# Kernel optimization log

Measured on AMD Instinct MI355X. Metric: run time of the kernel, lower is better.

## Reference

```python
import jax, jax.numpy as jnp
import numpy as np

C_M, C_Z, C_H = 256, 128, 32
EPS = 1e-3      # outer-product-mean normalization eps
LN_EPS = 1e-5   # LayerNorm eps (torch default)


def setup_inputs() -> dict:
    key = jax.random.key(0)
    ks = jax.random.split(key, 8)
    B, S, R = 1, 128, 256
    m = jax.random.normal(ks[0], (B, S, R, C_M), dtype=jnp.float32)
    mask = jnp.ones((B, S, R), dtype=jnp.float32)
    ln_g = jnp.ones((C_M,), dtype=jnp.float32)
    ln_b = jnp.zeros((C_M,), dtype=jnp.float32)
    w1 = jax.random.normal(ks[1], (C_M, C_H), dtype=jnp.float32) * (1.0 / np.sqrt(C_M))
    b1 = jnp.zeros((C_H,), dtype=jnp.float32)
    w2 = jax.random.normal(ks[2], (C_M, C_H), dtype=jnp.float32) * (1.0 / np.sqrt(C_M))
    b2 = jnp.zeros((C_H,), dtype=jnp.float32)
    # linear_out uses init='final' (zeros) in training; use small random for a nontrivial baseline
    w_out = jax.random.normal(ks[3], (C_H * C_H, C_Z), dtype=jnp.float32) * 0.02
    b_out = jnp.zeros((C_Z,), dtype=jnp.float32)
    return {"m": m, "mask": mask, "ln_g": ln_g, "ln_b": ln_b,
            "w1": w1, "b1": b1, "w2": w2, "b2": b2,
            "w_out": w_out, "b_out": b_out}


def reference(m, mask, ln_g, ln_b, w1, b1, w2, b2, w_out, b_out):
    # LayerNorm over c_m
    mu = jnp.mean(m, axis=-1, keepdims=True)
    var = jnp.mean(jnp.square(m - mu), axis=-1, keepdims=True)
    mn = (m - mu) * jax.lax.rsqrt(var + LN_EPS) * ln_g + ln_b

    msk = mask[..., None]                       # [B,S,R,1]
    a = (mn @ w1 + b1) * msk                    # [B,S,R,h]
    b = (mn @ w2 + b2) * msk                    # [B,S,R,h]
    a = jnp.swapaxes(a, -2, -3)                 # [B,R,S,h]
    b = jnp.swapaxes(b, -2, -3)                 # [B,R,S,h]

    # outer product mean over the MSA (seq) dim: [B,R,R,h,h]
    outer = jnp.einsum('...isc,...jse->...ijce', a, b)
    outer = outer.reshape(*outer.shape[:-2], C_H * C_H)  # [B,R,R,h*h]
    outer = outer @ w_out + b_out               # [B,R,R,c_z]

    # normalization: pairwise count of valid MSA rows
    norm = jnp.einsum('...sia,...sja->...ija', msk, msk)  # [B,R,R,1]
    return outer / (EPS + norm)
```

## Files before the change

### kernel.cpp

```cpp
#include <hip/hip_runtime.h>

#define R   256
#define S   128
#define CM  256
#define CH  32
#define CZ  128

typedef __attribute__((ext_vector_type(8))) short short8;
typedef __attribute__((ext_vector_type(4))) float f32x4;
typedef unsigned short ushort_t;

__device__ inline ushort_t f2bf(float f) {
    union { float f; unsigned u; } v; v.f = f;
    unsigned u = v.u;
    unsigned r = u + 0x7FFF + ((u >> 16) & 1);
    return (ushort_t)(r >> 16);
}

__global__ __launch_bounds__(256) void k_prep(
    const float* __restrict__ mask, const float* __restrict__ w_out,
    const float* __restrict__ w1, const float* __restrict__ w2,
    float* __restrict__ scale, ushort_t* __restrict__ WTp,
    ushort_t* __restrict__ WcatT) {
    int b = blockIdx.x, t = threadIdx.x;
    if (b < 256) {
        int i = b, j = t;
        float acc = 0.f;
        for (int s = 0; s < S; ++s) acc += mask[s * R + i] * mask[s * R + j];
        scale[i * R + j] = 1.0f / (1e-3f + acc);
    } else if (b < 384) {
        int z = b - 256;
        #pragma unroll
        for (int q = 0; q < 4; ++q) {
            int k2 = q * 256 + t;
            int e = k2 >> 5, c = k2 & 31;
            WTp[(size_t)z * 1024 + k2] = f2bf(w_out[(size_t)(c * 32 + e) * CZ + z]);
        }
    } else {
        int ch = b - 384, k = t;
        const float* w = (ch < CH) ? w1 : w2;
        WcatT[(size_t)ch * CM + k] = f2bf(w[(size_t)k * CH + (ch & 31)]);
    }
}

__global__ __launch_bounds__(256) void k_lnproj(
    const float* __restrict__ m, const float* __restrict__ mask,
    const float* __restrict__ g, const float* __restrict__ beta,
    const float* __restrict__ b1, const float* __restrict__ b2,
    const ushort_t* __restrict__ WcatT,
    ushort_t* __restrict__ Abig, ushort_t* __restrict__ BbigT) {
    __shared__ ushort_t mnL[64 * CM];
    __shared__ ushort_t wL[64 * CM];
    int t = threadIdx.x;
    int sg = blockIdx.x & 7, rg = blockIdx.x >> 3;
    int s0 = sg * 16, r0 = rg * 4;

    int ml = t >> 2, part = t & 3;
    int r_l = ml >> 4, s_l = ml & 15;
    size_t p = (size_t)(s0 + s_l) * R + (r0 + r_l);
    const float4* row = (const float4*)(m + p * CM + part * 64);
    float4 x[16];
    float sum = 0.f, sq = 0.f;
    #pragma unroll
    for (int i = 0; i < 16; ++i) {
        x[i] = row[i];
        sum += x[i].x + x[i].y + x[i].z + x[i].w;
        sq  += x[i].x * x[i].x + x[i].y * x[i].y
             + x[i].z * x[i].z + x[i].w * x[i].w;
    }
    sum += __shfl_xor(sum, 1); sum += __shfl_xor(sum, 2);
    sq  += __shfl_xor(sq, 1);  sq  += __shfl_xor(sq, 2);
    float mean = sum * (1.0f / CM);
    float var  = sq * (1.0f / CM) - mean * mean;
    float inv  = rsqrtf(var + 1e-5f);
    const float4* g4 = (const float4*)(g + part * 64);
    const float4* be4 = (const float4*)(beta + part * 64);
    #pragma unroll
    for (int c8 = 0; c8 < 8; ++c8) {
        float4 a = x[2 * c8], b = x[2 * c8 + 1];
        float4 ga = g4[2 * c8], gb = g4[2 * c8 + 1];
        float4 ba = be4[2 * c8], bb = be4[2 * c8 + 1];
        union { ushort_t u[8]; uint4 v; } pk;
        pk.u[0] = f2bf((a.x - mean) * inv * ga.x + ba.x);
        pk.u[1] = f2bf((a.y - mean) * inv * ga.y + ba.y);
        pk.u[2] = f2bf((a.z - mean) * inv * ga.z + ba.z);
        pk.u[3] = f2bf((a.w - mean) * inv * ga.w + ba.w);
        pk.u[4] = f2bf((b.x - mean) * inv * gb.x + bb.x);
        pk.u[5] = f2bf((b.y - mean) * inv * gb.y + bb.y);
        pk.u[6] = f2bf((b.z - mean) * inv * gb.z + bb.z);
        pk.u[7] = f2bf((b.w - mean) * inv * gb.w + bb.w);
        int ck = part * 8 + c8;
        int phys = ck ^ (ml & 15);
        *(uint4*)&mnL[ml * CM + phys * 8] = pk.v;
    }
    #pragma unroll
    for (int it = 0; it < 8; ++it) {
        int v = t + it * 256;
        int ch = v >> 5, ck = v & 31;
        int phys = ck ^ (ch & 15);
        *(uint4*)&wL[ch * CM + phys * 8] =
            *(const uint4*)&WcatT[(size_t)ch * CM + ck * 8];
    }
    __syncthreads();

    int w = t >> 6, lane = t & 63, quad = lane >> 4, l15 = lane & 15;
    int ch = w * 16 + l15;
    f32x4 acc[4];
    #pragma unroll
    for (int a = 0; a < 4; a++) acc[a] = (f32x4)(0.f);
    #pragma unroll
    for (int ks = 0; ks < 8; ++ks) {
        int cb = ks * 4 + quad;
        short8 bfr = *(const short8*)&wL[ch * CM + ((cb ^ l15) << 3)];
        #pragma unroll
        for (int mt = 0; mt < 4; ++mt) {
            int mm = mt * 16 + l15;
            short8 afr = *(const short8*)&mnL[mm * CM + ((cb ^ l15) << 3)];
            acc[mt] = __builtin_amdgcn_mfma_f32_16x16x32_bf16(afr, bfr, acc[mt], 0, 0, 0);
        }
    }

    int c = ch & 31;
    float bias = (ch < CH) ? b1[c] : b2[c];
    ushort_t* dst = (ch < CH) ? Abig : BbigT;
    #pragma unroll
    for (int mt = 0; mt < 4; ++mt) {
        int r = r0 + mt;
        union { ushort_t u[4]; uint2 v; } pk;
        #pragma unroll
        for (int reg = 0; reg < 4; ++reg) {
            int s = s0 + quad * 4 + reg;
            float mv = mask[(size_t)s * R + r];
            pk.u[reg] = f2bf((acc[mt][reg] + bias) * mv);
        }
        *(uint2*)&dst[((size_t)r * CH + c) * S + s0 + quad * 4] = pk.v;
    }
}

__global__ __launch_bounds__(512, 4) void k_fuse(
    const ushort_t* __restrict__ Abig, const ushort_t* __restrict__ BbigT,
    const ushort_t* __restrict__ WTp, const float* __restrict__ b_out,
    const float* __restrict__ scale, float* __restrict__ out) {
    __shared__ ushort_t oc[64 * 128];
    __shared__ ushort_t shB[2][32 * 128];
    int t = threadIdx.x;
    int w = t >> 6, lane = t & 63, quad = lane >> 4, l15 = lane & 15;
    int ib = blockIdx.x >> 5, jb = blockIdx.x & 31;
    int i_g = ib * 8 + w;
    int jj = l15 & 7, elb = l15 >> 3;

    short8 af[2][4];
    #pragma unroll
    for (int mt = 0; mt < 2; ++mt)
        #pragma unroll
        for (int ks = 0; ks < 4; ++ks)
            af[mt][ks] = *(const short8*)
                &Abig[((size_t)i_g * 32 + mt * 16 + l15) * S + ks * 32 + quad * 8];

    int r2 = t >> 4, ck = t & 15;
    const ushort_t* gB = BbigT
        + ((size_t)jb * 256 + (r2 & 7) * 32 + (r2 >> 3)) * S + ck * 8;
    ushort_t* bdst[2];
    bdst[0] = &shB[0][r2 * 128 + ((ck ^ (r2 & 15)) << 3)];
    bdst[1] = &shB[1][r2 * 128 + ((ck ^ (r2 & 15)) << 3)];
    uint4 breg = *(const uint4*)&gB[0];

    const ushort_t* Wp = WTp + (size_t)(w * 16 + l15) * 1024 + quad * 8;
    int pwr = w * 8 + jj;

    f32x4 acc2[4];
    #pragma unroll
    for (int pt = 0; pt < 4; ++pt) acc2[pt] = (f32x4)(0.f);

    for (int ec = 0; ec < 8; ++ec) {
        int buf = ec & 1;
        *(uint4*)bdst[buf] = breg;
        if (ec < 7) breg = *(const uint4*)&gB[(ec + 1) * 512];
        __syncthreads();

        f32x4 acc1[2][2];
        #pragma unroll
        for (int a = 0; a < 2; a++)
            #pragma unroll
            for (int b = 0; b < 2; b++) acc1[a][b] = (f32x4)(0.f);
        #pragma unroll
        for (int ks = 0; ks < 4; ++ks) {
            int chq = ks * 4 + quad;
            int r20 = elb * 8 + jj;
            int r21 = r20 + 16;
            short8 bf0 = *(const short8*)
                &shB[buf][r20 * 128 + ((chq ^ (r20 & 15)) << 3)];
            short8 bf1 = *(const short8*)
                &shB[buf][r21 * 128 + ((chq ^ (r21 & 15)) << 3)];
            #pragma unroll
            for (int mt = 0; mt < 2; ++mt) {
                acc1[mt][0] = __builtin_amdgcn_mfma_f32_16x16x32_bf16(
                    af[mt][ks], bf0, acc1[mt][0], 0, 0, 0);
                acc1[mt][1] = __builtin_amdgcn_mfma_f32_16x16x32_bf16(
                    af[mt][ks], bf1, acc1[mt][1], 0, 0, 0);
            }
        }
        #pragma unroll
        for (int mt = 0; mt < 2; ++mt) {
            int c00 = mt * 16 + quad * 4;
            #pragma unroll
            for (int nt = 0; nt < 2; ++nt) {
                int el = nt * 2 + elb;
                int k2l = el * 32 + c00;
                int cc = k2l >> 3;
                union { ushort_t u[4]; uint2 v; } pk;
                #pragma unroll
                for (int reg = 0; reg < 4; ++reg)
                    pk.u[reg] = f2bf(acc1[mt][nt][reg]);
                *(uint2*)((char*)oc + pwr * 256 + ((cc ^ (pwr & 7)) << 4)
                          + ((k2l & 7) << 1)) = pk.v;
            }
        }
        __syncthreads();
        #pragma unroll
        for (int ksl = 0; ksl < 4; ++ksl) {
            short8 wf = *(const short8*)&Wp[ec * 128 + ksl * 32];
            #pragma unroll
            for (int pt = 0; pt < 4; ++pt) {
                int pp = pt * 16 + l15;
                int cc = ksl * 4 + quad;
                short8 of = *(const short8*)
                    ((const char*)oc + pp * 256 + ((cc ^ (pp & 7)) << 4));
                acc2[pt] = __builtin_amdgcn_mfma_f32_16x16x32_bf16(
                    of, wf, acc2[pt], 0, 0, 0);
            }
        }
    }

    float bz = b_out[w * 16 + l15];
    #pragma unroll
    for (int pt = 0; pt < 4; ++pt) {
        #pragma unroll
        for (int reg = 0; reg < 4; ++reg) {
            int pp = pt * 16 + quad * 4 + reg;
            int pg = (ib * 8 + (pp >> 3)) * R + jb * 8 + (pp & 7);
            out[(size_t)pg * CZ + w * 16 + l15] = (acc2[pt][reg] + bz) * scale[pg];
        }
    }
}

extern "C" void kernel_launch(void* const* d_in, const int* in_sizes, int n_in,
                              void* d_out, int out_size, void* d_ws, size_t ws_size,
                              hipStream_t stream) {
    const float* m    = (const float*)d_in[0];
    const float* mask = (const float*)d_in[1];
    const float* g    = (const float*)d_in[2];
    const float* be   = (const float*)d_in[3];
    const float* w1   = (const float*)d_in[4];
    const float* b1   = (const float*)d_in[5];
    const float* w2   = (const float*)d_in[6];
    const float* b2   = (const float*)d_in[7];
    const float* wo   = (const float*)d_in[8];
    const float* bo   = (const float*)d_in[9];
    float* out = (float*)d_out;

    char* ws = (char*)d_ws;
    ushort_t* Abig  = (ushort_t*)ws;
    ushort_t* BbigT = Abig + (size_t)R * CH * S;
    ushort_t* WTp   = BbigT + (size_t)R * CH * S;
    ushort_t* WcatT = WTp + (size_t)CZ * CH * CH;
    float*    scale = (float*)(WcatT + (size_t)64 * CM);

    k_prep<<<448, 256, 0, stream>>>(mask, wo, w1, w2, scale, WTp, WcatT);
    k_lnproj<<<512, 256, 0, stream>>>(m, mask, g, be, b1, b2, WcatT, Abig, BbigT);
    k_fuse<<<1024, 512, 0, stream>>>(Abig, BbigT, WTp, bo, scale, out);
}
```

Before: 163.5 us.

## Split mask-count reduction across more blocks, register-load weights, prefetch W_out fragments

The pairwise mask-count prep is spread over four times as many blocks, each wave summing a quarter of the sequence with a shared-memory reduction, which shortens the serial 128-step loop. In the LayerNorm-projection kernel the weight tile is loaded straight from global into registers instead of staged through LDS, halving LDS use and dropping a copy. The fused outer-product kernel now prefetches the next chunk's W_out fragments into registers during the current iteration. The cost is higher register pressure, which may reduce occupancy.

```diff
diff --git a/kernel.cpp b/kernel.cpp
--- a/kernel.cpp
+++ b/kernel.cpp
@@ -22,14 +22,25 @@
     const float* __restrict__ w1, const float* __restrict__ w2,
     float* __restrict__ scale, ushort_t* __restrict__ WTp,
     ushort_t* __restrict__ WcatT) {
+    __shared__ float red[4][64];
     int b = blockIdx.x, t = threadIdx.x;
-    if (b < 256) {
-        int i = b, j = t;
+    if (b < 1024) {
+        int i = b >> 2, jq = b & 3;
+        int jl = t & 63, wv = t >> 6;
+        int j = jq * 64 + jl;
+        const float* mi = mask + (size_t)(wv * 32) * R + i;
+        const float* mj = mask + (size_t)(wv * 32) * R + j;
         float acc = 0.f;
-        for (int s = 0; s < S; ++s) acc += mask[s * R + i] * mask[s * R + j];
-        scale[i * R + j] = 1.0f / (1e-3f + acc);
-    } else if (b < 384) {
-        int z = b - 256;
+        #pragma unroll
+        for (int s = 0; s < 32; ++s) acc += mi[s * R] * mj[s * R];
+        red[wv][jl] = acc;
+        __syncthreads();
+        if (t < 64) {
+            float v = red[0][t] + red[1][t] + red[2][t] + red[3][t];
+            scale[(size_t)i * R + jq * 64 + t] = 1.0f / (1e-3f + v);
+        }
+    } else if (b < 1152) {
+        int z = b - 1024;
         #pragma unroll
         for (int q = 0; q < 4; ++q) {
             int k2 = q * 256 + t;
@@ -37,7 +48,7 @@
             WTp[(size_t)z * 1024 + k2] = f2bf(w_out[(size_t)(c * 32 + e) * CZ + z]);
         }
     } else {
-        int ch = b - 384, k = t;
+        int ch = b - 1152, k = t;
         const float* w = (ch < CH) ? w1 : w2;
         WcatT[(size_t)ch * CM + k] = f2bf(w[(size_t)k * CH + (ch & 31)]);
     }
@@ -50,7 +61,6 @@
     const ushort_t* __restrict__ WcatT,
     ushort_t* __restrict__ Abig, ushort_t* __restrict__ BbigT) {
     __shared__ ushort_t mnL[64 * CM];
-    __shared__ ushort_t wL[64 * CM];
     int t = threadIdx.x;
     int sg = blockIdx.x & 7, rg = blockIdx.x >> 3;
     int s0 = sg * 16, r0 = rg * 4;
@@ -93,30 +103,26 @@
         int phys = ck ^ (ml & 15);
         *(uint4*)&mnL[ml * CM + phys * 8] = pk.v;
     }
-    #pragma unroll
-    for (int it = 0; it < 8; ++it) {
-        int v = t + it * 256;
-        int ch = v >> 5, ck = v & 31;
-        int phys = ck ^ (ch & 15);
-        *(uint4*)&wL[ch * CM + phys * 8] =
-            *(const uint4*)&WcatT[(size_t)ch * CM + ck * 8];
-    }
-    __syncthreads();
 
     int w = t >> 6, lane = t & 63, quad = lane >> 4, l15 = lane & 15;
     int ch = w * 16 + l15;
+    short8 bfrs[8];
+    #pragma unroll
+    for (int ks = 0; ks < 8; ++ks)
+        bfrs[ks] = *(const short8*)&WcatT[(size_t)ch * CM + (ks * 4 + quad) * 8];
+    __syncthreads();
+
     f32x4 acc[4];
     #pragma unroll
     for (int a = 0; a < 4; a++) acc[a] = (f32x4)(0.f);
     #pragma unroll
     for (int ks = 0; ks < 8; ++ks) {
         int cb = ks * 4 + quad;
-        short8 bfr = *(const short8*)&wL[ch * CM + ((cb ^ l15) << 3)];
         #pragma unroll
         for (int mt = 0; mt < 4; ++mt) {
             int mm = mt * 16 + l15;
             short8 afr = *(const short8*)&mnL[mm * CM + ((cb ^ l15) << 3)];
-            acc[mt] = __builtin_amdgcn_mfma_f32_16x16x32_bf16(afr, bfr, acc[mt], 0, 0, 0);
+            acc[mt] = __builtin_amdgcn_mfma_f32_16x16x32_bf16(afr, bfrs[ks], acc[mt], 0, 0, 0);
         }
     }
 
@@ -166,6 +172,10 @@
     uint4 breg = *(const uint4*)&gB[0];
 
     const ushort_t* Wp = WTp + (size_t)(w * 16 + l15) * 1024 + quad * 8;
+    short8 wcur[4], wnxt[4];
+    #pragma unroll
+    for (int k = 0; k < 4; ++k) wcur[k] = *(const short8*)&Wp[k * 32];
+
     int pwr = w * 8 + jj;
 
     f32x4 acc2[4];
@@ -175,8 +185,14 @@
     for (int ec = 0; ec < 8; ++ec) {
         int buf = ec & 1;
         *(uint4*)bdst[buf] = breg;
-        if (ec < 7) breg = *(const uint4*)&gB[(ec + 1) * 512];
         __syncthreads();
+
+        if (ec < 7) {
+            breg = *(const uint4*)&gB[(ec + 1) * 512];
+            #pragma unroll
+            for (int k = 0; k < 4; ++k)
+                wnxt[k] = *(const short8*)&Wp[(ec + 1) * 128 + k * 32];
+        }
 
         f32x4 acc1[2][2];
         #pragma unroll
@@ -219,7 +235,7 @@
         __syncthreads();
         #pragma unroll
         for (int ksl = 0; ksl < 4; ++ksl) {
-            short8 wf = *(const short8*)&Wp[ec * 128 + ksl * 32];
+            short8 wf = wcur[ksl];
             #pragma unroll
             for (int pt = 0; pt < 4; ++pt) {
                 int pp = pt * 16 + l15;
@@ -230,6 +246,8 @@
                     of, wf, acc2[pt], 0, 0, 0);
             }
         }
+        #pragma unroll
+        for (int k = 0; k < 4; ++k) wcur[k] = wnxt[k];
     }
 
     float bz = b_out[w * 16 + l15];
@@ -266,7 +284,7 @@
     ushort_t* WcatT = WTp + (size_t)CZ * CH * CH;
     float*    scale = (float*)(WcatT + (size_t)64 * CM);
 
-    k_prep<<<448, 256, 0, stream>>>(mask, wo, w1, w2, scale, WTp, WcatT);
+    k_prep<<<1216, 256, 0, stream>>>(mask, wo, w1, w2, scale, WTp, WcatT);
     k_lnproj<<<512, 256, 0, stream>>>(m, mask, g, be, b1, b2, WcatT, Abig, BbigT);
     k_fuse<<<1024, 512, 0, stream>>>(Abig, BbigT, WTp, bo, scale, out);
 }
```

After: 158.3 us. -3.1%, faster.
